# Kernel tuning notes

Hardware: AMD Instinct MI355X
Metric: run time of the kernel (lower is better)

Reference implementation:

```python
import jax, jax.numpy as jnp
import numpy as np

NUM_HEADS = 8
NS = 27  # 3x3x3 deformable samples per query


def _resize1d(x, axis, new):
    # linear resize along one axis, align_corners=False (matches F.interpolate); identity if size matches
    old = x.shape[axis]
    if old == new:
        return x
    pos = (jnp.arange(new, dtype=jnp.float32) + 0.5) * (old / new) - 0.5
    f = jnp.floor(pos)
    w = pos - f
    i0 = jnp.clip(f, 0, old - 1).astype(jnp.int32)
    i1 = jnp.clip(f + 1, 0, old - 1).astype(jnp.int32)
    shp = [1] * x.ndim
    shp[axis] = new
    w = w.reshape(shp)
    return jnp.take(x, i0, axis=axis) * (1 - w) + jnp.take(x, i1, axis=axis) * w


def _rel_to_abs(x):
    # x: (b, d, h, w, w+NS-1) -> (b, d, h, w, NS) via the pad/reshape shifting trick
    b, d, h, w, c = x.shape
    x = jnp.pad(x, ((0, 0), (0, 0), (0, 0), (0, 0), (0, 1)))
    x = x.reshape(b, d, h, w * (c + 1))
    x = jnp.pad(x, ((0, 0), (0, 0), (0, 0), (0, NS - 1)))
    x = x.reshape(b, d, h, w + 1, NS + w - 1)
    return x[:, :, :, :w, w - 1:]


def _rel_logits_1d(q, rel_k):
    # q: (BH, 1, A, B, C, hd); rel_k: (C+NS-1, hd) -> (BH, A, B, C, NS)
    logits = jnp.einsum('nzxywd,rd->nzxywr', q, rel_k)
    n, z, a, b, c, r = logits.shape
    return _rel_to_abs(logits.reshape(n, z * a, b, c, r))


def _pos_emb(q, rel_depth, rel_height, rel_width, D, H, W):
    # q: (BH, 1, D, H, W, hd) -> (BH, D, H, W, NS)
    rw = _resize1d(rel_width, 0, W + NS - 1)
    rh = _resize1d(rel_height, 0, H + NS - 1)
    rd = _resize1d(rel_depth, 0, D + NS - 1)
    lw = _rel_logits_1d(q, rw)            # (BH, D, H, W, NS)
    qh = jnp.swapaxes(q, 3, 4)            # (BH, 1, D, W, H, hd)
    lh = _rel_logits_1d(qh, rh)           # (BH, D, W, H, NS)
    qd = jnp.swapaxes(qh, 2, 4)           # (BH, 1, H, W, D, hd)
    ld = _rel_logits_1d(qd, rd)           # (BH, H, W, D, NS)
    # trilinear resize of lh/ld to (D, H, W) over spatial axes (identity when D==H==W)
    for ax, tgt in ((1, D), (2, H), (3, W)):
        lh = _resize1d(lh, ax, tgt)
        ld = _resize1d(ld, ax, tgt)
    return lw + lh + ld


def _deform_unfold3d(x, offset):
    # x: (BH, C, D, H, W); offset: (BH, NS*3, D, H, W) -> (BH, C*NS, D*H*W)
    BH, C, D, H, W = x.shape
    off = offset.reshape(BH, NS, 3, D, H, W)
    k = jnp.arange(NS)
    kz = (k // 9 - 1).astype(jnp.float32)
    ky = (k // 3 % 3 - 1).astype(jnp.float32)
    kx = (k % 3 - 1).astype(jnp.float32)
    zz, yy, xx = jnp.meshgrid(jnp.arange(D, dtype=jnp.float32),
                              jnp.arange(H, dtype=jnp.float32),
                              jnp.arange(W, dtype=jnp.float32), indexing='ij')
    pz = zz + kz[:, None, None, None] + off[:, :, 0]   # (BH, NS, D, H, W)
    py = yy + ky[:, None, None, None] + off[:, :, 1]
    px = xx + kx[:, None, None, None] + off[:, :, 2]
    z0 = jnp.floor(pz); y0 = jnp.floor(py); x0 = jnp.floor(px)
    wz = pz - z0; wy = py - y0; wx = px - x0
    z0 = z0.astype(jnp.int32); y0 = y0.astype(jnp.int32); x0 = x0.astype(jnp.int32)
    S = D * H * W
    xf = x.reshape(BH, C, S)
    acc = jnp.zeros((BH, C, NS * S), dtype=x.dtype)
    for dz in (0, 1):
        for dy in (0, 1):
            for dx in (0, 1):
                zi = z0 + dz; yi = y0 + dy; xi = x0 + dx
                valid = ((zi >= 0) & (zi < D) & (yi >= 0) & (yi < H) & (xi >= 0) & (xi < W)).astype(x.dtype)
                w = (wz if dz else 1 - wz) * (wy if dy else 1 - wy) * (wx if dx else 1 - wx) * valid
                idx = (jnp.clip(zi, 0, D - 1) * H + jnp.clip(yi, 0, H - 1)) * W + jnp.clip(xi, 0, W - 1)
                g = jnp.take_along_axis(xf, idx.reshape(BH, 1, NS * S), axis=2)  # (BH, C, NS*S)
                acc = acc + g * w.reshape(BH, 1, NS * S)
    return acc.reshape(BH, C * NS, S)


def _forward(x, w_qkv, w_proj, b_proj, w_off, rel_depth, rel_height, rel_width, D, H, W):
    B, N, C = x.shape
    nh = NUM_HEADS
    hd = C // nh
    scale = hd ** -0.5
    BH = B * nh
    qkv = (x @ w_qkv.T).reshape(B, N, 3, nh, hd)
    q = qkv[:, :, 0].transpose(0, 2, 1, 3)  # (B, nh, N, hd)
    k = qkv[:, :, 1].transpose(0, 2, 1, 3)
    v = qkv[:, :, 2].transpose(0, 2, 1, 3)
    offset = (x.reshape(B, N, nh, hd) @ w_off.T).transpose(0, 2, 3, 1).reshape(BH, NS * 3, D, H, W)
    kmap = k.transpose(0, 1, 3, 2).reshape(BH, hd, D, H, W)
    vmap = v.transpose(0, 1, 3, 2).reshape(BH, hd, D, H, W)
    ks = _deform_unfold3d(kmap, offset).transpose(0, 2, 1).reshape(B, nh, N, hd, NS)
    vs = _deform_unfold3d(vmap, offset).reshape(B, nh, hd, NS, N).transpose(0, 1, 4, 3, 2)  # (B, nh, N, NS, hd)
    attn = jnp.einsum('bhnd,bhnds->bhns', q, ks) * scale
    pos = _pos_emb(q.reshape(BH, 1, D, H, W, hd), rel_depth, rel_height, rel_width, D, H, W).reshape(B, nh, N, NS)
    attn = jax.nn.softmax(attn + pos, axis=-1)
    out = jnp.einsum('bhns,bhnsd->bhnd', attn, vs).transpose(0, 2, 1, 3).reshape(B, N, C)
    return out @ w_proj.T + b_proj


def setup_inputs():
    key = jax.random.key(0)
    ks = jax.random.split(key, 8)
    B, D, H, W, C = 1, 16, 16, 16, 512
    N = D * H * W
    hd = C // NUM_HEADS
    return {
        'x': jax.random.normal(ks[0], (B, N, C), dtype=jnp.float32),
        'w_qkv': jax.random.normal(ks[1], (3 * C, C), dtype=jnp.float32) * 0.02,
        'w_proj': jax.random.normal(ks[2], (C, C), dtype=jnp.float32) * 0.02,
        'b_proj': jnp.zeros((C,), dtype=jnp.float32),
        'w_off': jax.random.normal(ks[3], (NS * 3, hd), dtype=jnp.float32) * 0.01,
        'rel_depth': jax.random.normal(ks[4], (D + NS - 1, hd), dtype=jnp.float32) * hd ** -0.5,
        'rel_height': jax.random.normal(ks[5], (H + NS - 1, hd), dtype=jnp.float32) * hd ** -0.5,
        'rel_width': jax.random.normal(ks[6], (W + NS - 1, hd), dtype=jnp.float32) * hd ** -0.5,
        'D': D, 'H': H, 'W': W,
    }


def reference(x, w_qkv, w_proj, b_proj, w_off, rel_depth, rel_height, rel_width, D, H, W):
    return _forward(x, w_qkv, w_proj, b_proj, w_off, rel_depth, rel_height, rel_width, D, H, W)
```

## Files before the change

kernel.cpp:

```cpp
#include <hip/hip_runtime.h>
#include <hip/hip_fp16.h>
#include <math.h>
#include <stdint.h>

#define NH    8
#define HD    64
#define NTOK  4096
#define CDIM  512
#define NSAMP 27

typedef __attribute__((ext_vector_type(8))) _Float16 half8;
typedef __attribute__((ext_vector_type(4))) float floatx4;
typedef unsigned short ushort_t;

__device__ __forceinline__ ushort_t f16b(float f) {
  return __half_as_ushort(__float2half(f));
}
__device__ __forceinline__ __half2 u2h2(uint32_t u) { return __builtin_bit_cast(__half2, u); }
__device__ __forceinline__ uint32_t h22u(__half2 h) { return __builtin_bit_cast(uint32_t, h); }

__device__ __forceinline__ float wave_sum_bcast(float x) {
#define DPP_STEP(ctrl, rmask)                                                   \
  { int t = __builtin_amdgcn_update_dpp(0, __float_as_int(x), ctrl, rmask, 0xf, \
                                        true);                                  \
    x += __int_as_float(t); }
  DPP_STEP(0x111, 0xf)
  DPP_STEP(0x112, 0xf)
  DPP_STEP(0x114, 0xf)
  DPP_STEP(0x118, 0xf)
  DPP_STEP(0x142, 0xa)
  DPP_STEP(0x143, 0xc)
#undef DPP_STEP
  return __int_as_float(__builtin_amdgcn_readlane(__float_as_int(x), 63));
}

__global__ __launch_bounds__(256) void k_cvt(const float* __restrict__ x,
                                             const float* __restrict__ wq,
                                             const float* __restrict__ wp,
                                             const float* __restrict__ w_off,
                                             const float* __restrict__ rel_d,
                                             const float* __restrict__ rel_h,
                                             const float* __restrict__ rel_w,
                                             ushort_t* __restrict__ xb,
                                             ushort_t* __restrict__ wqb,
                                             ushort_t* __restrict__ wpb,
                                             ushort_t* __restrict__ w_offh,
                                             ushort_t* __restrict__ relh) {
  int i = blockIdx.x * 256 + threadIdx.x;
  const float4* src = nullptr;
  ushort_t* dst;
  int off;
  float4 v = make_float4(0.f, 0.f, 0.f, 0.f);
  if (i < 524288)      { src = (const float4*)x;  dst = xb;  off = i; }
  else if (i < 720896) { src = (const float4*)wq; dst = wqb; off = i - 524288; }
  else if (i < 786432) { src = (const float4*)wp; dst = wpb; off = i - 720896; }
  else {
    int t = i - 786432;
    if (t < 2048) {
      off = t;
      int e = t * 4, row = e >> 6;
      if (row < 81) v = *(const float4*)&w_off[e];
      dst = w_offh;
    } else {
      off = t - 2048;
      int e = off * 4, row = e >> 6, col = e & 63;
      if (row < 42)       v = *(const float4*)&rel_w[row * 64 + col];
      else if (row < 84)  v = *(const float4*)&rel_h[(row - 42) * 64 + col];
      else if (row < 126) v = *(const float4*)&rel_d[(row - 84) * 64 + col];
      dst = relh;
    }
  }
  if (src) v = src[off];
  ushort4 o = make_ushort4(f16b(v.x), f16b(v.y), f16b(v.z), f16b(v.w));
  *(ushort4*)&dst[(size_t)off * 4] = o;
}

__global__ __launch_bounds__(256) void k_qkv(const ushort_t* __restrict__ Ah,
                                             const ushort_t* __restrict__ Bth,
                                             ushort_t* __restrict__ qh16,
                                             uint32_t* __restrict__ kvb) {
  __shared__ __align__(16) ushort_t As[64 * 32];
  __shared__ __align__(16) ushort_t Bs[128 * 32];
  __shared__ __align__(16) ushort_t Cs[64 * 136];
  const int tid = threadIdx.x;
  const int wave = tid >> 6, lane = tid & 63;
  const int wr = wave >> 1, wc = wave & 1;
  const int m15 = lane & 15, quad = lane >> 4;
  const int bm = blockIdx.x, bn = blockIdx.y;
  const bool is_q = (bn < 4);
  const int h = bn - 4;
  floatx4 acc[2][4];
#pragma unroll
  for (int i = 0; i < 2; i++)
#pragma unroll
    for (int j = 0; j < 4; j++) acc[i][j] = {0.f, 0.f, 0.f, 0.f};

  const int r0 = tid >> 2, c0 = (tid & 3) * 8;
  const int brA = is_q ? (bn * 128 + r0) : (512 + h * 64 + r0);
  const int brB = is_q ? (bn * 128 + 64 + r0) : (1024 + h * 64 + r0);
  for (int k0 = 0; k0 < 512; k0 += 32) {
    *(uint4*)&As[r0 * 32 + c0] = *(const uint4*)&Ah[(size_t)(bm * 64 + r0) * 512 + k0 + c0];
    *(uint4*)&Bs[r0 * 32 + c0]        = *(const uint4*)&Bth[(size_t)brA * 512 + k0 + c0];
    *(uint4*)&Bs[(r0 + 64) * 32 + c0] = *(const uint4*)&Bth[(size_t)brB * 512 + k0 + c0];
    __syncthreads();
    half8 af[2], bf[4];
#pragma unroll
    for (int i = 0; i < 2; i++)
      af[i] = *(const half8*)&As[(wr * 32 + i * 16 + m15) * 32 + quad * 8];
#pragma unroll
    for (int j = 0; j < 4; j++)
      bf[j] = *(const half8*)&Bs[(wc * 64 + j * 16 + m15) * 32 + quad * 8];
#pragma unroll
    for (int i = 0; i < 2; i++)
#pragma unroll
      for (int j = 0; j < 4; j++)
        acc[i][j] = __builtin_amdgcn_mfma_f32_16x16x32_f16(af[i], bf[j], acc[i][j], 0, 0, 0);
    __syncthreads();
  }

#pragma unroll
  for (int i = 0; i < 2; i++)
#pragma unroll
    for (int j = 0; j < 4; j++) {
      int col = wc * 64 + j * 16 + m15;
#pragma unroll
      for (int r = 0; r < 4; r++) {
        int row = wr * 32 + i * 16 + quad * 4 + r;
        Cs[row * 136 + col] = f16b(acc[i][j][r]);
      }
    }
  __syncthreads();

  if (is_q) {
#pragma unroll
    for (int it = 0; it < 4; it++) {
      int id = it * 256 + tid;
      int hh = id >> 9, row = (id >> 3) & 63, chunk = id & 7;
      uint4 d = *(const uint4*)&Cs[row * 136 + hh * 64 + chunk * 8];
      int hq = bn * 2 + hh;
      *(uint4*)&qh16[((size_t)hq * NTOK + bm * 64 + row) * 64 + chunk * 8] = d;
    }
  } else {
#pragma unroll
    for (int it = 0; it < 4; it++) {
      int id = it * 256 + tid;
      int row = id >> 4, chunk = id & 15;
      uint2 kk = *(const uint2*)&Cs[row * 136 + chunk * 4];
      uint2 vv = *(const uint2*)&Cs[row * 136 + 64 + chunk * 4];
      uint4 o;
      o.x = (kk.x & 0xffffu) | (vv.x << 16);
      o.y = (kk.x >> 16) | (vv.x & 0xffff0000u);
      o.z = (kk.y & 0xffffu) | (vv.y << 16);
      o.w = (kk.y >> 16) | (vv.y & 0xffff0000u);
      *(uint4*)&kvb[((size_t)h * NTOK + bm * 64 + row) * 64 + chunk * 4] = o;
    }
  }
}

__global__ __launch_bounds__(256) void k_aux(const ushort_t* __restrict__ xh,
                                             const ushort_t* __restrict__ qh16,
                                             const ushort_t* __restrict__ w_offh,
                                             const ushort_t* __restrict__ relh,
                                             float* __restrict__ ob,
                                             float* __restrict__ Pb) {
  __shared__ __align__(16) ushort_t As[128 * 32];
  __shared__ __align__(16) ushort_t Bs[128 * 32];
  const int tid = threadIdx.x;
  const int wave = tid >> 6, lane = tid & 63;
  const int wr = wave >> 1, wc = wave & 1;
  const int m15 = lane & 15, quad = lane >> 4;
  const int bm = blockIdx.x;
  const int mode = blockIdx.y >> 3, h = blockIdx.y & 7;

  const ushort_t* A;  int lda;
  const ushort_t* B;
  float* C;  int NC;
  if (mode == 0) { A = xh + h * 64;                  lda = 512; B = w_offh; C = ob + (size_t)h * NTOK * 81;  NC = 81; }
  else           { A = qh16 + (size_t)h * NTOK * 64; lda = 64;  B = relh;   C = Pb + (size_t)h * NTOK * 126; NC = 126; }

  floatx4 acc[4][4];
#pragma unroll
  for (int i = 0; i < 4; i++)
#pragma unroll
    for (int j = 0; j < 4; j++) acc[i][j] = {0.f, 0.f, 0.f, 0.f};

  const int r0 = tid >> 2, c0 = (tid & 3) * 8;
  const int r1 = r0 + 64;
  for (int k0 = 0; k0 < 64; k0 += 32) {
    *(uint4*)&As[r0 * 32 + c0] = *(const uint4*)&A[(size_t)(bm * 128 + r0) * lda + k0 + c0];
    *(uint4*)&As[r1 * 32 + c0] = *(const uint4*)&A[(size_t)(bm * 128 + r1) * lda + k0 + c0];
    *(uint4*)&Bs[r0 * 32 + c0] = *(const uint4*)&B[(size_t)r0 * 64 + k0 + c0];
    *(uint4*)&Bs[r1 * 32 + c0] = *(const uint4*)&B[(size_t)r1 * 64 + k0 + c0];
    __syncthreads();
    half8 af[4], bf[4];
#pragma unroll
    for (int i = 0; i < 4; i++)
      af[i] = *(const half8*)&As[(wr * 64 + i * 16 + m15) * 32 + quad * 8];
#pragma unroll
    for (int j = 0; j < 4; j++)
      bf[j] = *(const half8*)&Bs[(wc * 64 + j * 16 + m15) * 32 + quad * 8];
#pragma unroll
    for (int i = 0; i < 4; i++)
#pragma unroll
      for (int j = 0; j < 4; j++)
        acc[i][j] = __builtin_amdgcn_mfma_f32_16x16x32_f16(af[i], bf[j], acc[i][j], 0, 0, 0);
    __syncthreads();
  }

#pragma unroll
  for (int i = 0; i < 4; i++)
#pragma unroll
    for (int j = 0; j < 4; j++) {
      int col = wc * 64 + j * 16 + m15;
      if (col < NC) {
#pragma unroll
        for (int r = 0; r < 4; r++) {
          int row = bm * 128 + wr * 64 + i * 16 + quad * 4 + r;
          C[(size_t)row * NC + col] = acc[i][j][r];
        }
      }
    }
}

__global__ __launch_bounds__(256) void k_attn(const ushort_t* __restrict__ qh16,
                                              const uint32_t* __restrict__ kvb,
                                              const float* __restrict__ obuf,
                                              const float* __restrict__ Pbuf,
                                              ushort_t* __restrict__ attb16) {
  __shared__ int      s_off[4][NSAMP][8];
  __shared__ uint32_t s_cwh[4][NSAMP][8];
  __shared__ uint32_t vpair[4][14][64];
  __shared__ uint32_t s_wp[4][14];
  const int bid = blockIdx.x;
  const int h = bid & 7;
  const int wave = threadIdx.x >> 6;
  const int lane = threadIdx.x & 63;
  const int n = (bid >> 3) * 4 + wave;
  const int z = n >> 8, y = (n >> 4) & 15, xq = n & 15;
  const float qd = __half2float(__ushort_as_half(qh16[((size_t)h * NTOK + n) * 64 + lane]));
  const char* kvc = (const char*)(kvb + (size_t)h * NTOK * 64);
  const uint32_t lane4 = (uint32_t)lane * 4u;

  if (lane < NSAMP) {
    const int s = lane;
    const float* op = &obuf[((size_t)h * NTOK + n) * 81 + s * 3];
    float oz = op[0], oy = op[1], ox = op[2];
    float pz = (float)(z + (s / 9) - 1) + oz;
    float py = (float)(y + ((s / 3) % 3) - 1) + oy;
    float px = (float)(xq + (s % 3) - 1) + ox;
    float fz = floorf(pz), fy = floorf(py), fx = floorf(px);
    float wz = pz - fz, wy = py - fy, wx = px - fx;
    int z0 = (int)fz, y0 = (int)fy, x0 = (int)fx;
    int      oarr[8];
    uint32_t warr[8];
#pragma unroll
    for (int c = 0; c < 8; c++) {
      int dz = (c >> 2) & 1, dy = (c >> 1) & 1, dx = c & 1;
      int zi = z0 + dz, yi = y0 + dy, xi = x0 + dx;
      bool valid = (zi >= 0) && (zi < 16) && (yi >= 0) && (yi < 16) && (xi >= 0) && (xi < 16);
      float w = (dz ? wz : 1.f - wz) * (dy ? wy : 1.f - wy) * (dx ? wx : 1.f - wx);
      int zc = min(max(zi, 0), 15), yc = min(max(yi, 0), 15), xc = min(max(xi, 0), 15);
      oarr[c] = ((zc * 16 + yc) * 16 + xc) * 256;
      uint32_t hw = (uint32_t)f16b(valid ? w : 0.f);
      warr[c] = hw | (hw << 16);
    }
    *(int4*)&s_off[wave][s][0]  = make_int4(oarr[0], oarr[1], oarr[2], oarr[3]);
    *(int4*)&s_off[wave][s][4]  = make_int4(oarr[4], oarr[5], oarr[6], oarr[7]);
    *(uint4*)&s_cwh[wave][s][0] = make_uint4(warr[0], warr[1], warr[2], warr[3]);
    *(uint4*)&s_cwh[wave][s][4] = make_uint4(warr[4], warr[5], warr[6], warr[7]);
  }

  float mydot = 0.f;
  uint32_t prev_acc = 0;
#pragma unroll 2
  for (int s = 0; s < NSAMP; s++) {
    int4  o0 = *(const int4*)&s_off[wave][s][0];
    int4  o1 = *(const int4*)&s_off[wave][s][4];
    uint4 c0 = *(const uint4*)&s_cwh[wave][s][0];
    uint4 c1 = *(const uint4*)&s_cwh[wave][s][4];
    __half2 acc2 = u2h2(0u);
    uint32_t p;
#define CORNER(OV, WV)                                                       \
    p = *(const uint32_t*)(kvc + (uint32_t)((uint32_t)OV + lane4));          \
    acc2 = __hfma2(u2h2(WV), u2h2(p), acc2);
    CORNER(o0.x, c0.x) CORNER(o0.y, c0.y) CORNER(o0.z, c0.z) CORNER(o0.w, c0.w)
    CORNER(o1.x, c1.x) CORNER(o1.y, c1.y) CORNER(o1.z, c1.z) CORNER(o1.w, c1.w)
#undef CORNER
    float ak = __half2float(acc2.x);
    float tot = wave_sum_bcast(qd * ak);
    mydot = (lane == s) ? tot : mydot;
    uint32_t au = h22u(acc2);
    if (s & 1)
      vpair[wave][s >> 1][lane] = (prev_acc >> 16) | (au & 0xffff0000u);
    else
      prev_acc = au;
  }
  vpair[wave][13][lane] = prev_acc >> 16;

  float logit = -INFINITY;
  if (lane < NSAMP) {
    int j = 15 + lane - xq;
    int n2 = (z * 16 + xq) * 16 + y;
    int n3 = (xq * 16 + z) * 16 + y;
    float pos = Pbuf[((size_t)h * NTOK + n) * 126 + j]
              + Pbuf[((size_t)h * NTOK + n2) * 126 + 42 + j]
              + Pbuf[((size_t)h * NTOK + n3) * 126 + 84 + j];
    logit = mydot * 0.125f + pos;
  }

  float mx = logit;
#pragma unroll
  for (int off = 32; off >= 1; off >>= 1) mx = fmaxf(mx, __shfl_xor(mx, off, 64));
  float e = __expf(logit - mx);
  float sum = e;
#pragma unroll
  for (int off = 32; off >= 1; off >>= 1) sum += __shfl_xor(sum, off, 64);
  const float wgt = e / sum;
  uint32_t hw = (uint32_t)f16b(wgt);
  uint32_t nw = (uint32_t)__shfl_down((int)hw, 1, 64);
  if ((lane & 1) == 0 && lane < 28)
    s_wp[wave][lane >> 1] = hw | (nw << 16);

  __half2 out2 = u2h2(0u);
#pragma unroll
  for (int p2 = 0; p2 < 14; p2++) {
    __half2 v2 = u2h2(vpair[wave][p2][lane]);
    __half2 w2 = u2h2(s_wp[wave][p2]);
    out2 = __hfma2(w2, v2, out2);
  }
  float out = __half2float(out2.x) + __half2float(out2.y);
  attb16[(size_t)n * 512 + h * 64 + lane] = f16b(out);
}

__global__ __launch_bounds__(256) void k_proj(const ushort_t* __restrict__ Ah,
                                              const ushort_t* __restrict__ Bth,
                                              const float* __restrict__ bias,
                                              float* __restrict__ out) {
  __shared__ __align__(16) ushort_t As[64 * 32];
  __shared__ __align__(16) ushort_t Bs[64 * 32];
  const int tid = threadIdx.x;
  const int wave = tid >> 6, lane = tid & 63;
  const int wr = wave >> 1, wc = wave & 1;
  const int m15 = lane & 15, quad = lane >> 4;
  const int bm = blockIdx.x, bn = blockIdx.y;
  floatx4 acc[2][2];
#pragma unroll
  for (int i = 0; i < 2; i++)
#pragma unroll
    for (int j = 0; j < 2; j++) acc[i][j] = {0.f, 0.f, 0.f, 0.f};

  const int r0 = tid >> 2, c0 = (tid & 3) * 8;
  for (int k0 = 0; k0 < 512; k0 += 32) {
    *(uint4*)&As[r0 * 32 + c0] = *(const uint4*)&Ah[(size_t)(bm * 64 + r0) * 512 + k0 + c0];
    *(uint4*)&Bs[r0 * 32 + c0] = *(const uint4*)&Bth[(size_t)(bn * 64 + r0) * 512 + k0 + c0];
    __syncthreads();
    half8 af[2], bf[2];
#pragma unroll
    for (int i = 0; i < 2; i++)
      af[i] = *(const half8*)&As[(wr * 32 + i * 16 + m15) * 32 + quad * 8];
#pragma unroll
    for (int j = 0; j < 2; j++)
      bf[j] = *(const half8*)&Bs[(wc * 32 + j * 16 + m15) * 32 + quad * 8];
#pragma unroll
    for (int i = 0; i < 2; i++)
#pragma unroll
      for (int j = 0; j < 2; j++)
        acc[i][j] = __builtin_amdgcn_mfma_f32_16x16x32_f16(af[i], bf[j], acc[i][j], 0, 0, 0);
    __syncthreads();
  }

#pragma unroll
  for (int i = 0; i < 2; i++)
#pragma unroll
    for (int j = 0; j < 2; j++) {
      int col = bn * 64 + wc * 32 + j * 16 + m15;
      float b = bias[col];
#pragma unroll
      for (int r = 0; r < 4; r++) {
        int row = bm * 64 + wr * 32 + i * 16 + quad * 4 + r;
        out[(size_t)row * 512 + col] = acc[i][j][r] + b;
      }
    }
}

extern "C" void kernel_launch(void* const* d_in, const int* in_sizes, int n_in,
                              void* d_out, int out_size, void* d_ws, size_t ws_size,
                              hipStream_t stream) {
  const float* x      = (const float*)d_in[0];
  const float* w_qkv  = (const float*)d_in[1];
  const float* w_proj = (const float*)d_in[2];
  const float* b_proj = (const float*)d_in[3];
  const float* w_off  = (const float*)d_in[4];
  const float* rel_d  = (const float*)d_in[5];
  const float* rel_h  = (const float*)d_in[6];
  const float* rel_w  = (const float*)d_in[7];

  char* ws = (char*)d_ws;
  uint32_t* kvb    = (uint32_t*)ws; ws += (size_t)NH * NTOK * 64 * 4;
  float*    ob     = (float*)ws;    ws += (size_t)NH * NTOK * 81 * 4;
  float*    Pb     = (float*)ws;    ws += (size_t)NH * NTOK * 126 * 4;
  ushort_t* attb16 = (ushort_t*)ws; ws += (size_t)NTOK * CDIM * 2;
  ushort_t* xh     = (ushort_t*)ws; ws += (size_t)NTOK * CDIM * 2;
  ushort_t* wqh    = (ushort_t*)ws; ws += (size_t)3 * CDIM * CDIM * 2;
  ushort_t* wph    = (ushort_t*)ws; ws += (size_t)CDIM * CDIM * 2;
  ushort_t* qh16   = (ushort_t*)ws; ws += (size_t)NH * NTOK * 64 * 2;
  ushort_t* w_offh = (ushort_t*)ws; ws += (size_t)128 * 64 * 2;
  ushort_t* relh   = (ushort_t*)ws; ws += (size_t)128 * 64 * 2;
  float*    out    = (float*)d_out;

  k_cvt <<<dim3(3088), dim3(256), 0, stream>>>(x, w_qkv, w_proj, w_off, rel_d, rel_h,
                                               rel_w, xh, wqh, wph, w_offh, relh);
  k_qkv <<<dim3(64, 12), dim3(256), 0, stream>>>(xh, wqh, qh16, kvb);
  k_aux <<<dim3(32, 16), dim3(256), 0, stream>>>(xh, qh16, w_offh, relh, ob, Pb);
  k_attn<<<dim3(8192),   dim3(256), 0, stream>>>(qh16, kvb, ob, Pb, attb16);
  k_proj<<<dim3(64, 8),  dim3(256), 0, stream>>>(attb16, wph, b_proj, out);
}
```

Measured before the change: 174.9 us.

## Fuse fp32->fp16 conversion into GEMM loads and merge qkv/aux kernels into one launch

Drops the separate conversion kernel and converts fp32 inputs to fp16 while loading GEMM tiles. The qkv GEMM, offset GEMM and positional-logit GEMM become one kernel dispatched by block index. The positional-logit blocks recompute their head's Q projection locally instead of waiting on the qkv output, so the whole preprocessing needs no dependency between launches. This removes two launches and the fp16 staging buffers, at the cost of redundant Q computation and reading fp32 data (twice the bytes) inside the GEMM loops.

```diff
diff --git a/kernel.cpp b/kernel.cpp
--- a/kernel.cpp
+++ b/kernel.cpp
@@ -18,6 +18,17 @@
 }
 __device__ __forceinline__ __half2 u2h2(uint32_t u) { return __builtin_bit_cast(__half2, u); }
 __device__ __forceinline__ uint32_t h22u(__half2 h) { return __builtin_bit_cast(uint32_t, h); }
+
+__device__ __forceinline__ uint4 cvt8(const float* __restrict__ p) {
+  float4 a = *(const float4*)p;
+  float4 b = *(const float4*)(p + 4);
+  uint4 o;
+  o.x = (uint32_t)f16b(a.x) | ((uint32_t)f16b(a.y) << 16);
+  o.y = (uint32_t)f16b(a.z) | ((uint32_t)f16b(a.w) << 16);
+  o.z = (uint32_t)f16b(b.x) | ((uint32_t)f16b(b.y) << 16);
+  o.w = (uint32_t)f16b(b.z) | ((uint32_t)f16b(b.w) << 16);
+  return o;
+}
 
 __device__ __forceinline__ float wave_sum_bcast(float x) {
 #define DPP_STEP(ctrl, rmask)                                                   \
@@ -34,192 +45,231 @@
   return __int_as_float(__builtin_amdgcn_readlane(__float_as_int(x), 63));
 }
 
-__global__ __launch_bounds__(256) void k_cvt(const float* __restrict__ x,
-                                             const float* __restrict__ wq,
-                                             const float* __restrict__ wp,
+__global__ __launch_bounds__(256) void k_pre(const float* __restrict__ x,
+                                             const float* __restrict__ w_qkv,
                                              const float* __restrict__ w_off,
                                              const float* __restrict__ rel_d,
                                              const float* __restrict__ rel_h,
                                              const float* __restrict__ rel_w,
-                                             ushort_t* __restrict__ xb,
-                                             ushort_t* __restrict__ wqb,
-                                             ushort_t* __restrict__ wpb,
-                                             ushort_t* __restrict__ w_offh,
-                                             ushort_t* __restrict__ relh) {
-  int i = blockIdx.x * 256 + threadIdx.x;
-  const float4* src = nullptr;
-  ushort_t* dst;
-  int off;
-  float4 v = make_float4(0.f, 0.f, 0.f, 0.f);
-  if (i < 524288)      { src = (const float4*)x;  dst = xb;  off = i; }
-  else if (i < 720896) { src = (const float4*)wq; dst = wqb; off = i - 524288; }
-  else if (i < 786432) { src = (const float4*)wp; dst = wpb; off = i - 720896; }
-  else {
-    int t = i - 786432;
-    if (t < 2048) {
-      off = t;
-      int e = t * 4, row = e >> 6;
-      if (row < 81) v = *(const float4*)&w_off[e];
-      dst = w_offh;
-    } else {
-      off = t - 2048;
-      int e = off * 4, row = e >> 6, col = e & 63;
-      if (row < 42)       v = *(const float4*)&rel_w[row * 64 + col];
-      else if (row < 84)  v = *(const float4*)&rel_h[(row - 42) * 64 + col];
-      else if (row < 126) v = *(const float4*)&rel_d[(row - 84) * 64 + col];
-      dst = relh;
-    }
-  }
-  if (src) v = src[off];
-  ushort4 o = make_ushort4(f16b(v.x), f16b(v.y), f16b(v.z), f16b(v.w));
-  *(ushort4*)&dst[(size_t)off * 4] = o;
-}
-
-__global__ __launch_bounds__(256) void k_qkv(const ushort_t* __restrict__ Ah,
-                                             const ushort_t* __restrict__ Bth,
                                              ushort_t* __restrict__ qh16,
-                                             uint32_t* __restrict__ kvb) {
-  __shared__ __align__(16) ushort_t As[64 * 32];
-  __shared__ __align__(16) ushort_t Bs[128 * 32];
-  __shared__ __align__(16) ushort_t Cs[64 * 136];
+                                             uint32_t* __restrict__ kvb,
+                                             float* __restrict__ ob,
+                                             float* __restrict__ Pb) {
+  __shared__ __align__(16) char smem[36864];
   const int tid = threadIdx.x;
   const int wave = tid >> 6, lane = tid & 63;
   const int wr = wave >> 1, wc = wave & 1;
   const int m15 = lane & 15, quad = lane >> 4;
-  const int bm = blockIdx.x, bn = blockIdx.y;
-  const bool is_q = (bn < 4);
-  const int h = bn - 4;
-  floatx4 acc[2][4];
-#pragma unroll
-  for (int i = 0; i < 2; i++)
-#pragma unroll
-    for (int j = 0; j < 4; j++) acc[i][j] = {0.f, 0.f, 0.f, 0.f};
-
+  const int bid = blockIdx.x;
   const int r0 = tid >> 2, c0 = (tid & 3) * 8;
-  const int brA = is_q ? (bn * 128 + r0) : (512 + h * 64 + r0);
-  const int brB = is_q ? (bn * 128 + 64 + r0) : (1024 + h * 64 + r0);
-  for (int k0 = 0; k0 < 512; k0 += 32) {
-    *(uint4*)&As[r0 * 32 + c0] = *(const uint4*)&Ah[(size_t)(bm * 64 + r0) * 512 + k0 + c0];
-    *(uint4*)&Bs[r0 * 32 + c0]        = *(const uint4*)&Bth[(size_t)brA * 512 + k0 + c0];
-    *(uint4*)&Bs[(r0 + 64) * 32 + c0] = *(const uint4*)&Bth[(size_t)brB * 512 + k0 + c0];
+
+  if (bid < 768) {
+    const int bm = bid & 63, bn = bid >> 6;
+    const bool is_q = (bn < 4);
+    const int h = bn - 4;
+    ushort_t* As = (ushort_t*)smem;
+    ushort_t* Bs = (ushort_t*)(smem + 4096);
+    ushort_t* Cs = (ushort_t*)(smem + 4096 + 8192);
+    floatx4 acc[2][4];
+#pragma unroll
+    for (int i = 0; i < 2; i++)
+#pragma unroll
+      for (int j = 0; j < 4; j++) acc[i][j] = {0.f, 0.f, 0.f, 0.f};
+
+    const int brA = is_q ? (bn * 128 + r0) : (512 + h * 64 + r0);
+    const int brB = is_q ? (bn * 128 + 64 + r0) : (1024 + h * 64 + r0);
+    for (int k0 = 0; k0 < 512; k0 += 32) {
+      *(uint4*)&As[r0 * 32 + c0] = cvt8(&x[(size_t)(bm * 64 + r0) * 512 + k0 + c0]);
+      *(uint4*)&Bs[r0 * 32 + c0]        = cvt8(&w_qkv[(size_t)brA * 512 + k0 + c0]);
+      *(uint4*)&Bs[(r0 + 64) * 32 + c0] = cvt8(&w_qkv[(size_t)brB * 512 + k0 + c0]);
+      __syncthreads();
+      half8 af[2], bf[4];
+#pragma unroll
+      for (int i = 0; i < 2; i++)
+        af[i] = *(const half8*)&As[(wr * 32 + i * 16 + m15) * 32 + quad * 8];
+#pragma unroll
+      for (int j = 0; j < 4; j++)
+        bf[j] = *(const half8*)&Bs[(wc * 64 + j * 16 + m15) * 32 + quad * 8];
+#pragma unroll
+      for (int i = 0; i < 2; i++)
+#pragma unroll
+        for (int j = 0; j < 4; j++)
+          acc[i][j] = __builtin_amdgcn_mfma_f32_16x16x32_f16(af[i], bf[j], acc[i][j], 0, 0, 0);
+      __syncthreads();
+    }
+#pragma unroll
+    for (int i = 0; i < 2; i++)
+#pragma unroll
+      for (int j = 0; j < 4; j++) {
+        int col = wc * 64 + j * 16 + m15;
+#pragma unroll
+        for (int r = 0; r < 4; r++) {
+          int row = wr * 32 + i * 16 + quad * 4 + r;
+          Cs[row * 136 + col] = f16b(acc[i][j][r]);
+        }
+      }
     __syncthreads();
-    half8 af[2], bf[4];
-#pragma unroll
-    for (int i = 0; i < 2; i++)
-      af[i] = *(const half8*)&As[(wr * 32 + i * 16 + m15) * 32 + quad * 8];
-#pragma unroll
-    for (int j = 0; j < 4; j++)
-      bf[j] = *(const half8*)&Bs[(wc * 64 + j * 16 + m15) * 32 + quad * 8];
-#pragma unroll
-    for (int i = 0; i < 2; i++)
+    if (is_q) {
+#pragma unroll
+      for (int it = 0; it < 4; it++) {
+        int id = it * 256 + tid;
+        int hh = id >> 9, row = (id >> 3) & 63, chunk = id & 7;
+        uint4 d = *(const uint4*)&Cs[row * 136 + hh * 64 + chunk * 8];
+        int hq = bn * 2 + hh;
+        *(uint4*)&qh16[((size_t)hq * NTOK + bm * 64 + row) * 64 + chunk * 8] = d;
+      }
+    } else {
+#pragma unroll
+      for (int it = 0; it < 4; it++) {
+        int id = it * 256 + tid;
+        int row = id >> 4, chunk = id & 15;
+        uint2 kk = *(const uint2*)&Cs[row * 136 + chunk * 4];
+        uint2 vv = *(const uint2*)&Cs[row * 136 + 64 + chunk * 4];
+        uint4 o;
+        o.x = (kk.x & 0xffffu) | (vv.x << 16);
+        o.y = (kk.x >> 16) | (vv.x & 0xffff0000u);
+        o.z = (kk.y & 0xffffu) | (vv.y << 16);
+        o.w = (kk.y >> 16) | (vv.y & 0xffff0000u);
+        *(uint4*)&kvb[((size_t)h * NTOK + bm * 64 + row) * 64 + chunk * 4] = o;
+      }
+    }
+  } else if (bid < 1024) {
+    const int b2 = bid - 768;
+    const int bm = b2 & 31, h = b2 >> 5;
+    ushort_t* As = (ushort_t*)smem;
+    ushort_t* Bs = (ushort_t*)(smem + 8192);
+    floatx4 acc[4][4];
+#pragma unroll
+    for (int i = 0; i < 4; i++)
+#pragma unroll
+      for (int j = 0; j < 4; j++) acc[i][j] = {0.f, 0.f, 0.f, 0.f};
+    const int r1 = r0 + 64;
+    const uint4 z4 = {0u, 0u, 0u, 0u};
+    for (int k0 = 0; k0 < 64; k0 += 32) {
+      *(uint4*)&As[r0 * 32 + c0] = cvt8(&x[(size_t)(bm * 128 + r0) * 512 + h * 64 + k0 + c0]);
+      *(uint4*)&As[r1 * 32 + c0] = cvt8(&x[(size_t)(bm * 128 + r1) * 512 + h * 64 + k0 + c0]);
+      *(uint4*)&Bs[r0 * 32 + c0] = (r0 < 81) ? cvt8(&w_off[r0 * 64 + k0 + c0]) : z4;
+      *(uint4*)&Bs[r1 * 32 + c0] = (r1 < 81) ? cvt8(&w_off[r1 * 64 + k0 + c0]) : z4;
+      __syncthreads();
+      half8 af[4], bf[4];
+#pragma unroll
+      for (int i = 0; i < 4; i++)
+        af[i] = *(const half8*)&As[(wr * 64 + i * 16 + m15) * 32 + quad * 8];
 #pragma unroll
       for (int j = 0; j < 4; j++)
-        acc[i][j] = __builtin_amdgcn_mfma_f32_16x16x32_f16(af[i], bf[j], acc[i][j], 0, 0, 0);
+        bf[j] = *(const half8*)&Bs[(wc * 64 + j * 16 + m15) * 32 + quad * 8];
+#pragma unroll
+      for (int i = 0; i < 4; i++)
+#pragma unroll
+        for (int j = 0; j < 4; j++)
+          acc[i][j] = __builtin_amdgcn_mfma_f32_16x16x32_f16(af[i], bf[j], acc[i][j], 0, 0, 0);
+      __syncthreads();
+    }
+#pragma unroll
+    for (int i = 0; i < 4; i++)
+#pragma unroll
+      for (int j = 0; j < 4; j++) {
+        int col = wc * 64 + j * 16 + m15;
+        if (col < 81) {
+#pragma unroll
+          for (int r = 0; r < 4; r++) {
+            int row = bm * 128 + wr * 64 + i * 16 + quad * 4 + r;
+            ob[((size_t)h * NTOK + row) * 81 + col] = acc[i][j][r];
+          }
+        }
+      }
+  } else {
+    const int b2 = bid - 1024;
+    const int bm = b2 & 31, h = b2 >> 5;
+    ushort_t* Qs = (ushort_t*)smem;
+    ushort_t* As = (ushort_t*)(smem + 18432);
+    ushort_t* Bq = (ushort_t*)(smem + 18432 + 8192);
+    ushort_t* Br = (ushort_t*)(smem + 18432);
+    const int r1 = r0 + 64;
+
+    floatx4 qacc[4][2];
+#pragma unroll
+    for (int i = 0; i < 4; i++)
+#pragma unroll
+      for (int j = 0; j < 2; j++) qacc[i][j] = {0.f, 0.f, 0.f, 0.f};
+    for (int k0 = 0; k0 < 512; k0 += 32) {
+      *(uint4*)&As[r0 * 32 + c0] = cvt8(&x[(size_t)(bm * 128 + r0) * 512 + k0 + c0]);
+      *(uint4*)&As[r1 * 32 + c0] = cvt8(&x[(size_t)(bm * 128 + r1) * 512 + k0 + c0]);
+      *(uint4*)&Bq[r0 * 32 + c0] = cvt8(&w_qkv[(size_t)(h * 64 + r0) * 512 + k0 + c0]);
+      __syncthreads();
+      half8 af[4], bf[2];
+#pragma unroll
+      for (int i = 0; i < 4; i++)
+        af[i] = *(const half8*)&As[(wr * 64 + i * 16 + m15) * 32 + quad * 8];
+#pragma unroll
+      for (int j = 0; j < 2; j++)
+        bf[j] = *(const half8*)&Bq[(wc * 32 + j * 16 + m15) * 32 + quad * 8];
+#pragma unroll
+      for (int i = 0; i < 4; i++)
+#pragma unroll
+        for (int j = 0; j < 2; j++)
+          qacc[i][j] = __builtin_amdgcn_mfma_f32_16x16x32_f16(af[i], bf[j], qacc[i][j], 0, 0, 0);
+      __syncthreads();
+    }
+#pragma unroll
+    for (int i = 0; i < 4; i++)
+#pragma unroll
+      for (int j = 0; j < 2; j++) {
+        int col = wc * 32 + j * 16 + m15;
+#pragma unroll
+        for (int r = 0; r < 4; r++) {
+          int row = wr * 64 + i * 16 + quad * 4 + r;
+          Qs[row * 72 + col] = f16b(qacc[i][j][r]);
+        }
+      }
+    const uint4 z4 = {0u, 0u, 0u, 0u};
+#pragma unroll
+    for (int kk = 0; kk < 64; kk += 32) {
+#pragma unroll
+      for (int half = 0; half < 2; half++) {
+        int rr = r0 + half * 64;
+        uint4 v = z4;
+        if (rr < 42)       v = cvt8(&rel_w[rr * 64 + kk + c0]);
+        else if (rr < 84)  v = cvt8(&rel_h[(rr - 42) * 64 + kk + c0]);
+        else if (rr < 126) v = cvt8(&rel_d[(rr - 84) * 64 + kk + c0]);
+        *(uint4*)&Br[rr * 72 + kk + c0] = v;
+      }
+    }
     __syncthreads();
-  }
-
-#pragma unroll
-  for (int i = 0; i < 2; i++)
-#pragma unroll
-    for (int j = 0; j < 4; j++) {
-      int col = wc * 64 + j * 16 + m15;
-#pragma unroll
-      for (int r = 0; r < 4; r++) {
-        int row = wr * 32 + i * 16 + quad * 4 + r;
-        Cs[row * 136 + col] = f16b(acc[i][j][r]);
-      }
-    }
-  __syncthreads();
-
-  if (is_q) {
-#pragma unroll
-    for (int it = 0; it < 4; it++) {
-      int id = it * 256 + tid;
-      int hh = id >> 9, row = (id >> 3) & 63, chunk = id & 7;
-      uint4 d = *(const uint4*)&Cs[row * 136 + hh * 64 + chunk * 8];
-      int hq = bn * 2 + hh;
-      *(uint4*)&qh16[((size_t)hq * NTOK + bm * 64 + row) * 64 + chunk * 8] = d;
-    }
-  } else {
-#pragma unroll
-    for (int it = 0; it < 4; it++) {
-      int id = it * 256 + tid;
-      int row = id >> 4, chunk = id & 15;
-      uint2 kk = *(const uint2*)&Cs[row * 136 + chunk * 4];
-      uint2 vv = *(const uint2*)&Cs[row * 136 + 64 + chunk * 4];
-      uint4 o;
-      o.x = (kk.x & 0xffffu) | (vv.x << 16);
-      o.y = (kk.x >> 16) | (vv.x & 0xffff0000u);
-      o.z = (kk.y & 0xffffu) | (vv.y << 16);
-      o.w = (kk.y >> 16) | (vv.y & 0xffff0000u);
-      *(uint4*)&kvb[((size_t)h * NTOK + bm * 64 + row) * 64 + chunk * 4] = o;
-    }
-  }
-}
-
-__global__ __launch_bounds__(256) void k_aux(const ushort_t* __restrict__ xh,
-                                             const ushort_t* __restrict__ qh16,
-                                             const ushort_t* __restrict__ w_offh,
-                                             const ushort_t* __restrict__ relh,
-                                             float* __restrict__ ob,
-                                             float* __restrict__ Pb) {
-  __shared__ __align__(16) ushort_t As[128 * 32];
-  __shared__ __align__(16) ushort_t Bs[128 * 32];
-  const int tid = threadIdx.x;
-  const int wave = tid >> 6, lane = tid & 63;
-  const int wr = wave >> 1, wc = wave & 1;
-  const int m15 = lane & 15, quad = lane >> 4;
-  const int bm = blockIdx.x;
-  const int mode = blockIdx.y >> 3, h = blockIdx.y & 7;
-
-  const ushort_t* A;  int lda;
-  const ushort_t* B;
-  float* C;  int NC;
-  if (mode == 0) { A = xh + h * 64;                  lda = 512; B = w_offh; C = ob + (size_t)h * NTOK * 81;  NC = 81; }
-  else           { A = qh16 + (size_t)h * NTOK * 64; lda = 64;  B = relh;   C = Pb + (size_t)h * NTOK * 126; NC = 126; }
-
-  floatx4 acc[4][4];
-#pragma unroll
-  for (int i = 0; i < 4; i++)
-#pragma unroll
-    for (int j = 0; j < 4; j++) acc[i][j] = {0.f, 0.f, 0.f, 0.f};
-
-  const int r0 = tid >> 2, c0 = (tid & 3) * 8;
-  const int r1 = r0 + 64;
-  for (int k0 = 0; k0 < 64; k0 += 32) {
-    *(uint4*)&As[r0 * 32 + c0] = *(const uint4*)&A[(size_t)(bm * 128 + r0) * lda + k0 + c0];
-    *(uint4*)&As[r1 * 32 + c0] = *(const uint4*)&A[(size_t)(bm * 128 + r1) * lda + k0 + c0];
-    *(uint4*)&Bs[r0 * 32 + c0] = *(const uint4*)&B[(size_t)r0 * 64 + k0 + c0];
-    *(uint4*)&Bs[r1 * 32 + c0] = *(const uint4*)&B[(size_t)r1 * 64 + k0 + c0];
-    __syncthreads();
-    half8 af[4], bf[4];
-#pragma unroll
-    for (int i = 0; i < 4; i++)
-      af[i] = *(const half8*)&As[(wr * 64 + i * 16 + m15) * 32 + quad * 8];
-#pragma unroll
-    for (int j = 0; j < 4; j++)
-      bf[j] = *(const half8*)&Bs[(wc * 64 + j * 16 + m15) * 32 + quad * 8];
-#pragma unroll
-    for (int i = 0; i < 4; i++)
+    floatx4 pacc[4][4];
+#pragma unroll
+    for (int i = 0; i < 4; i++)
+#pragma unroll
+      for (int j = 0; j < 4; j++) pacc[i][j] = {0.f, 0.f, 0.f, 0.f};
+#pragma unroll
+    for (int kk = 0; kk < 64; kk += 32) {
+      half8 af[4], bf[4];
+#pragma unroll
+      for (int i = 0; i < 4; i++)
+        af[i] = *(const half8*)&Qs[(wr * 64 + i * 16 + m15) * 72 + kk + quad * 8];
 #pragma unroll
       for (int j = 0; j < 4; j++)
-        acc[i][j] = __builtin_amdgcn_mfma_f32_16x16x32_f16(af[i], bf[j], acc[i][j], 0, 0, 0);
-    __syncthreads();
-  }
-
-#pragma unroll
-  for (int i = 0; i < 4; i++)
-#pragma unroll
-    for (int j = 0; j < 4; j++) {
-      int col = wc * 64 + j * 16 + m15;
-      if (col < NC) {
-#pragma unroll
-        for (int r = 0; r < 4; r++) {
-          int row = bm * 128 + wr * 64 + i * 16 + quad * 4 + r;
-          C[(size_t)row * NC + col] = acc[i][j][r];
+        bf[j] = *(const half8*)&Br[(wc * 64 + j * 16 + m15) * 72 + kk + quad * 8];
+#pragma unroll
+      for (int i = 0; i < 4; i++)
+#pragma unroll
+        for (int j = 0; j < 4; j++)
+          pacc[i][j] = __builtin_amdgcn_mfma_f32_16x16x32_f16(af[i], bf[j], pacc[i][j], 0, 0, 0);
+    }
+#pragma unroll
+    for (int i = 0; i < 4; i++)
+#pragma unroll
+      for (int j = 0; j < 4; j++) {
+        int col = wc * 64 + j * 16 + m15;
+        if (col < 126) {
+#pragma unroll
+          for (int r = 0; r < 4; r++) {
+            int row = bm * 128 + wr * 64 + i * 16 + quad * 4 + r;
+            Pb[((size_t)h * NTOK + row) * 126 + col] = pacc[i][j][r];
+          }
         }
       }
-    }
+  }
 }
 
 __global__ __launch_bounds__(256) void k_attn(const ushort_t* __restrict__ qh16,
@@ -333,7 +383,7 @@
 }
 
 __global__ __launch_bounds__(256) void k_proj(const ushort_t* __restrict__ Ah,
-                                              const ushort_t* __restrict__ Bth,
+                                              const float* __restrict__ Wp,
                                               const float* __restrict__ bias,
                                               float* __restrict__ out) {
   __shared__ __align__(16) ushort_t As[64 * 32];
@@ -352,7 +402,7 @@
   const int r0 = tid >> 2, c0 = (tid & 3) * 8;
   for (int k0 = 0; k0 < 512; k0 += 32) {
     *(uint4*)&As[r0 * 32 + c0] = *(const uint4*)&Ah[(size_t)(bm * 64 + r0) * 512 + k0 + c0];
-    *(uint4*)&Bs[r0 * 32 + c0] = *(const uint4*)&Bth[(size_t)(bn * 64 + r0) * 512 + k0 + c0];
+    *(uint4*)&Bs[r0 * 32 + c0] = cvt8(&Wp[(size_t)(bn * 64 + r0) * 512 + k0 + c0]);
     __syncthreads();
     half8 af[2], bf[2];
 #pragma unroll
@@ -400,18 +450,11 @@
   float*    ob     = (float*)ws;    ws += (size_t)NH * NTOK * 81 * 4;
   float*    Pb     = (float*)ws;    ws += (size_t)NH * NTOK * 126 * 4;
   ushort_t* attb16 = (ushort_t*)ws; ws += (size_t)NTOK * CDIM * 2;
-  ushort_t* xh     = (ushort_t*)ws; ws += (size_t)NTOK * CDIM * 2;
-  ushort_t* wqh    = (ushort_t*)ws; ws += (size_t)3 * CDIM * CDIM * 2;
-  ushort_t* wph    = (ushort_t*)ws; ws += (size_t)CDIM * CDIM * 2;
   ushort_t* qh16   = (ushort_t*)ws; ws += (size_t)NH * NTOK * 64 * 2;
-  ushort_t* w_offh = (ushort_t*)ws; ws += (size_t)128 * 64 * 2;
-  ushort_t* relh   = (ushort_t*)ws; ws += (size_t)128 * 64 * 2;
   float*    out    = (float*)d_out;
 
-  k_cvt <<<dim3(3088), dim3(256), 0, stream>>>(x, w_qkv, w_proj, w_off, rel_d, rel_h,
-                                               rel_w, xh, wqh, wph, w_offh, relh);
-  k_qkv <<<dim3(64, 12), dim3(256), 0, stream>>>(xh, wqh, qh16, kvb);
-  k_aux <<<dim3(32, 16), dim3(256), 0, stream>>>(xh, qh16, w_offh, relh, ob, Pb);
-  k_attn<<<dim3(8192),   dim3(256), 0, stream>>>(qh16, kvb, ob, Pb, attb16);
-  k_proj<<<dim3(64, 8),  dim3(256), 0, stream>>>(attb16, wph, b_proj, out);
-}
+  k_pre <<<dim3(1280),  dim3(256), 0, stream>>>(x, w_qkv, w_off, rel_d, rel_h, rel_w,
+                                                qh16, kvb, ob, Pb);
+  k_attn<<<dim3(8192),  dim3(256), 0, stream>>>(qh16, kvb, ob, Pb, attb16);
+  k_proj<<<dim3(64, 8), dim3(256), 0, stream>>>(attb16, w_proj, b_proj, out);
+}
```

New measurement: 187.6 us. 7.3% more time.

## Process two queries per wave in deformable attention with 8-byte gathers

Applied to the files above, without the earlier changes.

Each wave now handles two query tokens, one per 32-lane half. Each lane loads 8 bytes (two k/v pairs) per corner, so the grid halves. The dot-product reduction stops at the half-wave and uses a ds_bpermute to broadcast instead of a readlane. Sampled values stay in a register array rather than being staged through shared memory, which removes the vpair LDS traffic but raises register pressure from the fully unrolled 27-sample loop.

```diff
diff --git a/kernel.cpp b/kernel.cpp
--- a/kernel.cpp
+++ b/kernel.cpp
@@ -19,7 +19,7 @@
 __device__ __forceinline__ __half2 u2h2(uint32_t u) { return __builtin_bit_cast(__half2, u); }
 __device__ __forceinline__ uint32_t h22u(__half2 h) { return __builtin_bit_cast(uint32_t, h); }
 
-__device__ __forceinline__ float wave_sum_bcast(float x) {
+__device__ __forceinline__ float half_sum_31_63(float x) {
 #define DPP_STEP(ctrl, rmask)                                                   \
   { int t = __builtin_amdgcn_update_dpp(0, __float_as_int(x), ctrl, rmask, 0xf, \
                                         true);                                  \
@@ -29,9 +29,8 @@
   DPP_STEP(0x114, 0xf)
   DPP_STEP(0x118, 0xf)
   DPP_STEP(0x142, 0xa)
-  DPP_STEP(0x143, 0xc)
 #undef DPP_STEP
-  return __int_as_float(__builtin_amdgcn_readlane(__float_as_int(x), 63));
+  return x;
 }
 
 __global__ __launch_bounds__(256) void k_cvt(const float* __restrict__ x,
@@ -227,22 +226,24 @@
                                               const float* __restrict__ obuf,
                                               const float* __restrict__ Pbuf,
                                               ushort_t* __restrict__ attb16) {
-  __shared__ int      s_off[4][NSAMP][8];
-  __shared__ uint32_t s_cwh[4][NSAMP][8];
-  __shared__ uint32_t vpair[4][14][64];
-  __shared__ uint32_t s_wp[4][14];
+  __shared__ __align__(16) int      s_off[4][2][NSAMP][8];
+  __shared__ __align__(16) uint32_t s_cwh[4][2][NSAMP][8];
+  __shared__ uint32_t s_wp[4][2][NSAMP];
   const int bid = blockIdx.x;
   const int h = bid & 7;
   const int wave = threadIdx.x >> 6;
   const int lane = threadIdx.x & 63;
-  const int n = (bid >> 3) * 4 + wave;
+  const int half = lane >> 5, il = lane & 31;
+  const int n = (bid >> 3) * 8 + wave * 2 + half;
   const int z = n >> 8, y = (n >> 4) & 15, xq = n & 15;
-  const float qd = __half2float(__ushort_as_half(qh16[((size_t)h * NTOK + n) * 64 + lane]));
+  __half2 qh2 = u2h2(*(const uint32_t*)&qh16[((size_t)h * NTOK + n) * 64 + il * 2]);
+  const float qdA = __half2float(qh2.x), qdB = __half2float(qh2.y);
   const char* kvc = (const char*)(kvb + (size_t)h * NTOK * 64);
-  const uint32_t lane4 = (uint32_t)lane * 4u;
-
-  if (lane < NSAMP) {
-    const int s = lane;
+  const uint32_t il8 = (uint32_t)il * 8u;
+  const int bsrc = ((lane & 32) | 31) << 2;
+
+  if (il < NSAMP) {
+    const int s = il;
     const float* op = &obuf[((size_t)h * NTOK + n) * 81 + s * 3];
     float oz = op[0], oy = op[1], ox = op[2];
     float pz = (float)(z + (s / 9) - 1) + oz;
@@ -264,42 +265,40 @@
       uint32_t hw = (uint32_t)f16b(valid ? w : 0.f);
       warr[c] = hw | (hw << 16);
     }
-    *(int4*)&s_off[wave][s][0]  = make_int4(oarr[0], oarr[1], oarr[2], oarr[3]);
-    *(int4*)&s_off[wave][s][4]  = make_int4(oarr[4], oarr[5], oarr[6], oarr[7]);
-    *(uint4*)&s_cwh[wave][s][0] = make_uint4(warr[0], warr[1], warr[2], warr[3]);
-    *(uint4*)&s_cwh[wave][s][4] = make_uint4(warr[4], warr[5], warr[6], warr[7]);
+    *(int4*)&s_off[wave][half][s][0]  = make_int4(oarr[0], oarr[1], oarr[2], oarr[3]);
+    *(int4*)&s_off[wave][half][s][4]  = make_int4(oarr[4], oarr[5], oarr[6], oarr[7]);
+    *(uint4*)&s_cwh[wave][half][s][0] = make_uint4(warr[0], warr[1], warr[2], warr[3]);
+    *(uint4*)&s_cwh[wave][half][s][4] = make_uint4(warr[4], warr[5], warr[6], warr[7]);
   }
 
   float mydot = 0.f;
-  uint32_t prev_acc = 0;
-#pragma unroll 2
+  __half2 vcache[NSAMP];
+#pragma unroll
   for (int s = 0; s < NSAMP; s++) {
-    int4  o0 = *(const int4*)&s_off[wave][s][0];
-    int4  o1 = *(const int4*)&s_off[wave][s][4];
-    uint4 c0 = *(const uint4*)&s_cwh[wave][s][0];
-    uint4 c1 = *(const uint4*)&s_cwh[wave][s][4];
-    __half2 acc2 = u2h2(0u);
-    uint32_t p;
+    int4  o0 = *(const int4*)&s_off[wave][half][s][0];
+    int4  o1 = *(const int4*)&s_off[wave][half][s][4];
+    uint4 c0 = *(const uint4*)&s_cwh[wave][half][s][0];
+    uint4 c1 = *(const uint4*)&s_cwh[wave][half][s][4];
+    __half2 a0 = u2h2(0u), a1 = u2h2(0u);
+    uint2 p2;
 #define CORNER(OV, WV)                                                       \
-    p = *(const uint32_t*)(kvc + (uint32_t)((uint32_t)OV + lane4));          \
-    acc2 = __hfma2(u2h2(WV), u2h2(p), acc2);
+    p2 = *(const uint2*)(kvc + (uint32_t)((uint32_t)OV + il8));              \
+    a0 = __hfma2(u2h2(WV), u2h2(p2.x), a0);                                  \
+    a1 = __hfma2(u2h2(WV), u2h2(p2.y), a1);
     CORNER(o0.x, c0.x) CORNER(o0.y, c0.y) CORNER(o0.z, c0.z) CORNER(o0.w, c0.w)
     CORNER(o1.x, c1.x) CORNER(o1.y, c1.y) CORNER(o1.z, c1.z) CORNER(o1.w, c1.w)
 #undef CORNER
-    float ak = __half2float(acc2.x);
-    float tot = wave_sum_bcast(qd * ak);
-    mydot = (lane == s) ? tot : mydot;
-    uint32_t au = h22u(acc2);
-    if (s & 1)
-      vpair[wave][s >> 1][lane] = (prev_acc >> 16) | (au & 0xffff0000u);
-    else
-      prev_acc = au;
-  }
-  vpair[wave][13][lane] = prev_acc >> 16;
+    float part = qdA * __half2float(a0.x) + qdB * __half2float(a1.x);
+    float red = half_sum_31_63(part);
+    int tot = __builtin_amdgcn_ds_bpermute(bsrc, __float_as_int(red));
+    mydot = (il == s) ? __int_as_float(tot) : mydot;
+    __half2 vc; vc.x = a0.y; vc.y = a1.y;
+    vcache[s] = vc;
+  }
 
   float logit = -INFINITY;
-  if (lane < NSAMP) {
-    int j = 15 + lane - xq;
+  if (il < NSAMP) {
+    int j = 15 + il - xq;
     int n2 = (z * 16 + xq) * 16 + y;
     int n3 = (xq * 16 + z) * 16 + y;
     float pos = Pbuf[((size_t)h * NTOK + n) * 126 + j]
@@ -310,26 +309,20 @@
 
   float mx = logit;
 #pragma unroll
-  for (int off = 32; off >= 1; off >>= 1) mx = fmaxf(mx, __shfl_xor(mx, off, 64));
+  for (int off = 16; off >= 1; off >>= 1) mx = fmaxf(mx, __shfl_xor(mx, off, 64));
   float e = __expf(logit - mx);
   float sum = e;
 #pragma unroll
-  for (int off = 32; off >= 1; off >>= 1) sum += __shfl_xor(sum, off, 64);
+  for (int off = 16; off >= 1; off >>= 1) sum += __shfl_xor(sum, off, 64);
   const float wgt = e / sum;
   uint32_t hw = (uint32_t)f16b(wgt);
-  uint32_t nw = (uint32_t)__shfl_down((int)hw, 1, 64);
-  if ((lane & 1) == 0 && lane < 28)
-    s_wp[wave][lane >> 1] = hw | (nw << 16);
+  if (il < NSAMP) s_wp[wave][half][il] = hw | (hw << 16);
 
   __half2 out2 = u2h2(0u);
 #pragma unroll
-  for (int p2 = 0; p2 < 14; p2++) {
-    __half2 v2 = u2h2(vpair[wave][p2][lane]);
-    __half2 w2 = u2h2(s_wp[wave][p2]);
-    out2 = __hfma2(w2, v2, out2);
-  }
-  float out = __half2float(out2.x) + __half2float(out2.y);
-  attb16[(size_t)n * 512 + h * 64 + lane] = f16b(out);
+  for (int s = 0; s < NSAMP; s++)
+    out2 = __hfma2(u2h2(s_wp[wave][half][s]), vcache[s], out2);
+  *(uint32_t*)&attb16[(size_t)n * 512 + h * 64 + il * 2] = h22u(out2);
 }
 
 __global__ __launch_bounds__(256) void k_proj(const ushort_t* __restrict__ Ah,
@@ -412,6 +405,6 @@
                                                rel_w, xh, wqh, wph, w_offh, relh);
   k_qkv <<<dim3(64, 12), dim3(256), 0, stream>>>(xh, wqh, qh16, kvb);
   k_aux <<<dim3(32, 16), dim3(256), 0, stream>>>(xh, qh16, w_offh, relh, ob, Pb);
-  k_attn<<<dim3(8192),   dim3(256), 0, stream>>>(qh16, kvb, ob, Pb, attb16);
-  k_proj<<<dim3(64, 8),  dim3(256), 0, stream>>>(attb16, wph, b_proj, out);
-}
+  k_attn<<<dim3(4096),   dim3(256), 0, stream>>>(qh16, kvb, ob, Pb, attb16);
+  k_proj<<<dim3(64, 8),  dim3(256), 0, stream>>>(attb16, w_proj ? (const ushort_t*)wph : wph, b_proj, out);
+}
```

Result: slower. 216.6 us (+23.8%).
